# Performance work log

Measured on AMD Instinct MI355X. Metric: run time of the kernel, lower is better.

## Reference

```python
import jax, jax.numpy as jnp
import numpy as np

B, T, E, H = 8, 2048, 1024, 128

def setup_inputs() -> dict:
    key = jax.random.key(0)
    kx, kq, kk, kv = jax.random.split(key, 4)
    return {
        "X": jax.random.normal(kx, (B, T, E), dtype=jnp.float32),
        "Wq": jax.random.normal(kq, (E, H), dtype=jnp.float32) * (E ** -0.5),
        "Wk": jax.random.normal(kk, (E, H), dtype=jnp.float32) * (E ** -0.5),
        "Wv": jax.random.normal(kv, (E, H), dtype=jnp.float32) * (E ** -0.5),
    }

def reference(X, Wq, Wk, Wv):
    # X: [B, T, E]; Wq/Wk/Wv: [E, H]
    q = X @ Wq  # [B, T, H]
    k = X @ Wk  # [B, T, H]
    v = X @ Wv  # [B, T, H]
    t = X.shape[1]
    scale = float(X.shape[-1]) ** 0.5  # NOTE: source scales by sqrt(embedding_size)
    w = jnp.einsum("bqh,bkh->bqk", q, k) / scale  # [B, T, T]
    mask = jnp.tril(jnp.ones((t, t), dtype=bool))  # causal tril buffer
    w = jnp.where(mask[None, :, :], w, -jnp.inf)
    # NOTE: source applies softmax over dim=1 (the query axis), faithfully reproduced
    w = jax.nn.softmax(w, axis=1)
    # dropout p=0.0 -> identity
    return jnp.einsum("bqk,bkh->bqh", w, v)  # [B, T, H]
```

## Files before the change

### kernel.cpp

```cpp
#include <hip/hip_runtime.h>
#include <hip/hip_bf16.h>
#include <stdint.h>

#define B_ 8
#define T_ 2048
#define E_ 1024
#define H_ 128
#define BT_ (B_*T_)

typedef unsigned short u16;
typedef unsigned int u32;
typedef __attribute__((ext_vector_type(4))) unsigned short u16x4;
typedef __attribute__((ext_vector_type(8))) short short8;
typedef __attribute__((ext_vector_type(4))) float f32x4;

#define MFMA_BF16(a,b,c) __builtin_amdgcn_mfma_f32_16x16x32_bf16((a),(b),(c),0,0,0)

__device__ __forceinline__ u16 bf16u(float f) {
  union { float f; unsigned u; } v; v.f = f;
  unsigned r = v.u + 0x7FFFu + ((v.u >> 16) & 1u);
  return (u16)(r >> 16);
}
__device__ __forceinline__ float ubf16(u16 u) {
  union { unsigned u; float f; } v; v.u = ((unsigned)u) << 16; return v.f;
}

__device__ __forceinline__ void gl16(const void* g, void* l) {
  __builtin_amdgcn_global_load_lds(
      (const __attribute__((address_space(1))) void*)g,
      (__attribute__((address_space(3))) void*)l, 16, 0, 0);
}

template<int R, int CB, bool SWZ>
__device__ __forceinline__ void stage_tile(const char* g, int gstride, char* lds) {
  const int lane = threadIdx.x & 63;
  const int wid  = threadIdx.x >> 6;
  constexpr int LPR   = CB / 16;
  constexpr int RPC   = 1024 / CB;
  constexpr int CALLS = (R * CB) / 1024;
  constexpr int CPW   = CALLS / 4;
#pragma unroll
  for (int c = 0; c < CPW; ++c) {
    const int call = wid * CPW + c;
    const int r0   = call * RPC;
    const int row  = r0 + lane / LPR;
    int s = lane % LPR;
    if (SWZ) s = s ^ (row & 7);
    gl16(g + (size_t)row * gstride + s * 16, lds + (size_t)r0 * CB);
  }
}

__device__ __forceinline__ short8 fragr(const u16* lds, int row, int colu16, int CBu) {
  const int slot = (colu16 >> 3) ^ (row & 7);
  return *(const short8*)&lds[(size_t)row * CBu + (slot << 3)];
}

__global__ void k_convert_x(const float* __restrict__ X, u16* __restrict__ Xb) {
  const int n4 = BT_ * E_ / 4;
  for (int i = blockIdx.x * 256 + threadIdx.x; i < n4; i += gridDim.x * 256) {
    float4 v = ((const float4*)X)[i];
    u16x4 o;
    o.x = bf16u(v.x); o.y = bf16u(v.y); o.z = bf16u(v.z); o.w = bf16u(v.w);
    ((u16x4*)Xb)[i] = o;
  }
}

__global__ void k_build_wt(const float* __restrict__ Wq, const float* __restrict__ Wk,
                           const float* __restrict__ Wv, u16* __restrict__ Wt) {
  int idx = blockIdx.x * 256 + threadIdx.x;
  if (idx >= 384 * 1024) return;
  int r = idx >> 10;
  int e = idx & 1023;
  int i = r >> 7;
  int h = r & 127;
  const float* W = (i == 0) ? Wq : (i == 1) ? Wk : Wv;
  float v = W[(size_t)e * 128 + h];
  if (i == 0) v *= 0.03125f;
  Wt[idx] = bf16u(v);
}

__global__ __launch_bounds__(256) void k_qkv_gemm(const u16* __restrict__ Xb, const u16* __restrict__ Wt,
                                                  u16* __restrict__ Qs, u16* __restrict__ Kb,
                                                  u16* __restrict__ Vt) {
  __shared__ __align__(16) u16 As[128 * 64];
  __shared__ __align__(16) u16 Bs[128 * 64];
  const int m0   = blockIdx.x * 128;
  const int nsel = blockIdx.y;
  const int n0   = nsel * 128;
  const int lane = threadIdx.x & 63;
  const int wid  = threadIdx.x >> 6;
  const int ln = lane & 15, hi = lane >> 4;
  const int wm = (wid >> 1) * 64, wn = (wid & 1) * 64;
  f32x4 acc[4][4] = {};
  for (int ks = 0; ks < E_; ks += 64) {
    stage_tile<128, 128, true>((const char*)(Xb + (size_t)m0 * E_ + ks), E_ * 2, (char*)As);
    stage_tile<128, 128, true>((const char*)(Wt + (size_t)n0 * E_ + ks), E_ * 2, (char*)Bs);
    __syncthreads();
#pragma unroll
    for (int kk = 0; kk < 2; ++kk) {
      short8 a[4], b[4];
#pragma unroll
      for (int mf = 0; mf < 4; ++mf)
        a[mf] = fragr(As, wm + mf * 16 + ln, kk * 32 + hi * 8, 64);
#pragma unroll
      for (int nf = 0; nf < 4; ++nf)
        b[nf] = fragr(Bs, wn + nf * 16 + ln, kk * 32 + hi * 8, 64);
#pragma unroll
      for (int mf = 0; mf < 4; ++mf)
#pragma unroll
        for (int nf = 0; nf < 4; ++nf)
          acc[mf][nf] = MFMA_BF16(a[mf], b[nf], acc[mf][nf]);
    }
    __syncthreads();
  }
#pragma unroll
  for (int mf = 0; mf < 4; ++mf)
#pragma unroll
    for (int nf = 0; nf < 4; ++nf)
#pragma unroll
      for (int i = 0; i < 4; ++i) {
        int r = m0 + wm + mf * 16 + hi * 4 + i;
        int c = wn + nf * 16 + ln;
        u16 u = bf16u(acc[mf][nf][i]);
        if (nsel == 0)      Qs[(size_t)r * H_ + c] = u;
        else if (nsel == 1) Kb[(size_t)r * H_ + c] = u;
        else {
          int bb = r >> 11, t = r & (T_ - 1);
          Vt[((size_t)bb * H_ + c) * T_ + t] = u;
        }
      }
}

__global__ __launch_bounds__(256) void k_score(const u16* __restrict__ Qs, const u16* __restrict__ Kb,
                                               u16* __restrict__ P, float* __restrict__ colsum,
                                               int b_base) {
  __shared__ __align__(16) u16 QtPs[128 * 128];
  __shared__ __align__(16) u16 Ks[128 * 128];
  __shared__ float cs[128];
  const int tid = blockIdx.x;
  const int bl  = blockIdx.y;
  const int b   = b_base + bl;
  int qt = (int)((sqrtf(8.f * tid + 1.f) - 1.f) * 0.5f);
  while ((qt + 1) * (qt + 2) / 2 <= tid) ++qt;
  while (qt * (qt + 1) / 2 > tid) --qt;
  const int kt = tid - qt * (qt + 1) / 2;

  const int lane = threadIdx.x & 63, wid = threadIdx.x >> 6;
  const int ln = lane & 15, hi = lane >> 4;
  const int wq0 = wid * 32;

  stage_tile<128, 256, true>((const char*)(Qs + ((size_t)b * T_ + qt * 128) * H_), H_ * 2, (char*)QtPs);
  stage_tile<128, 256, true>((const char*)(Kb + ((size_t)b * T_ + kt * 128) * H_), H_ * 2, (char*)Ks);
  if (threadIdx.x < 128) cs[threadIdx.x] = 0.f;
  __syncthreads();

  f32x4 acc[2][8] = {};
#pragma unroll
  for (int kk = 0; kk < 4; ++kk) {
    short8 a[2], bf[8];
#pragma unroll
    for (int mf = 0; mf < 2; ++mf)
      a[mf] = fragr(QtPs, wq0 + mf * 16 + ln, kk * 32 + hi * 8, 128);
#pragma unroll
    for (int nf = 0; nf < 8; ++nf)
      bf[nf] = fragr(Ks, nf * 16 + ln, kk * 32 + hi * 8, 128);
#pragma unroll
    for (int mf = 0; mf < 2; ++mf)
#pragma unroll
      for (int nf = 0; nf < 8; ++nf)
        acc[mf][nf] = MFMA_BF16(a[mf], bf[nf], acc[mf][nf]);
  }

  const bool diag = (qt == kt);
#pragma unroll
  for (int nf = 0; nf < 8; ++nf) {
    float s = 0.f;
    const int k = nf * 16 + ln;
#pragma unroll
    for (int mf = 0; mf < 2; ++mf) {
#pragma unroll
      for (int i = 0; i < 4; ++i) {
        const int q = wq0 + mf * 16 + hi * 4 + i;
        float w = __expf(acc[mf][nf][i]);
        if (diag && q < k) w = 0.f;
        acc[mf][nf][i] = w;
        s += w;
      }
    }
    s += __shfl_xor(s, 16);
    s += __shfl_xor(s, 32);
    if (hi == 0) atomicAdd(&cs[nf * 16 + ln], s);
  }
  __syncthreads();

  u16* Ps = QtPs;
  const bool evenlane = !(ln & 1);
#pragma unroll
  for (int mf = 0; mf < 2; ++mf)
#pragma unroll
    for (int nf = 0; nf < 8; ++nf) {
      f32x4 v = acc[mf][nf];
      f32x4 pv;
#pragma unroll
      for (int i = 0; i < 4; ++i) pv[i] = __shfl_xor(v[i], 1);
#pragma unroll
      for (int j = 0; j < 2; ++j) {
        const int i = evenlane ? j : (2 + j);
        const float lo = evenlane ? v[i] : pv[i];
        const float hh = evenlane ? pv[i] : v[i];
        const u32 pk = (u32)bf16u(lo) | ((u32)bf16u(hh) << 16);
        const int row = wq0 + mf * 16 + hi * 4 + i;
        const int kc  = nf * 16 + (ln & ~1);
        const int byt = row * 256 + ((((kc >> 3) ^ (row & 7)) << 4) | ((kc & 7) << 1));
        *(u32*)((char*)Ps + byt) = pk;
      }
    }
  __syncthreads();

  u16* ptile = P + (((size_t)bl * 136 + tid) << 14);
#pragma unroll
  for (int pass = 0; pass < 8; ++pass) {
    const int row = pass * 16 + (threadIdx.x >> 4);
    const int s   = threadIdx.x & 15;
    short8 val = *(const short8*)&Ps[row * 128 + (((s ^ (row & 7)) << 3))];
    *(short8*)&ptile[row * 128 + s * 8] = val;
  }
  if (threadIdx.x < 128)
    atomicAdd(&colsum[(size_t)b * T_ + kt * 128 + threadIdx.x], cs[threadIdx.x]);
}

__global__ void k_finalize_v(const float* __restrict__ colsum, u16* __restrict__ Vt, int b_base) {
  const int i8 = blockIdx.x * 256 + threadIdx.x;
  const int bl = i8 >> 15;
  const int r  = i8 & 32767;
  const int h  = r >> 8;
  const int t8 = r & 255;
  const int b  = b_base + bl;
  u16* p = Vt + ((size_t)b * H_ + h) * T_ + t8 * 8;
  const float* csp = colsum + (size_t)b * T_ + t8 * 8;
  short8 v = *(short8*)p;
  short8 o;
#pragma unroll
  for (int j = 0; j < 8; ++j) {
    float f = ubf16((u16)v[j]) / csp[j];
    o[j] = (short)bf16u(f);
  }
  *(short8*)p = o;
}

__global__ __launch_bounds__(256) void k_pv(const u16* __restrict__ P, const u16* __restrict__ Vt,
                                            float* __restrict__ out, int b_base) {
  __shared__ __align__(16) u16 Pt[128 * 128];
  __shared__ __align__(16) u16 Vs[128 * 128];
  const int id = blockIdx.x;
  const int bl = blockIdx.y;
  const int b  = b_base + bl;
  int qt = 0, cum = 0;
#pragma unroll
  for (int j = 0; j < 16; ++j) {
    const int n = (j + 2) >> 1;
    if (id < cum + n) { qt = j; break; }
    cum += n;
  }
  const int c   = id - cum;
  const int nch = (qt + 2) >> 1;
  const int kt0 = c * (qt + 1) / nch;
  const int kt1 = (c + 1) * (qt + 1) / nch;

  const int lane = threadIdx.x & 63, wid = threadIdx.x >> 6;
  const int ln = lane & 15, hi = lane >> 4;
  const int wq0 = wid * 32;

  f32x4 acc[2][8] = {};
  for (int kt = kt0; kt < kt1; ++kt) {
    const u16* ptile = P + (((size_t)bl * 136 + (size_t)qt * (qt + 1) / 2 + kt) << 14);
    stage_tile<128, 256, true>((const char*)ptile, 256, (char*)Pt);
    stage_tile<128, 256, true>((const char*)(Vt + (size_t)b * H_ * T_ + kt * 128), T_ * 2, (char*)Vs);
    __syncthreads();
#pragma unroll
    for (int kk = 0; kk < 4; ++kk) {
      short8 a[2], bf[8];
#pragma unroll
      for (int mf = 0; mf < 2; ++mf)
        a[mf] = fragr(Pt, wq0 + mf * 16 + ln, kk * 32 + hi * 8, 128);
#pragma unroll
      for (int nf = 0; nf < 8; ++nf)
        bf[nf] = fragr(Vs, nf * 16 + ln, kk * 32 + hi * 8, 128);
#pragma unroll
      for (int mf = 0; mf < 2; ++mf)
#pragma unroll
        for (int nf = 0; nf < 8; ++nf)
          acc[mf][nf] = MFMA_BF16(a[mf], bf[nf], acc[mf][nf]);
    }
    __syncthreads();
  }
#pragma unroll
  for (int mf = 0; mf < 2; ++mf)
#pragma unroll
    for (int nf = 0; nf < 8; ++nf)
#pragma unroll
      for (int i = 0; i < 4; ++i) {
        const int q = qt * 128 + wq0 + mf * 16 + hi * 4 + i;
        const int h = nf * 16 + ln;
        atomicAdd(&out[((size_t)b * T_ + q) * H_ + h], acc[mf][nf][i]);
      }
}

extern "C" void kernel_launch(void* const* d_in, const int* in_sizes, int n_in,
                              void* d_out, int out_size, void* d_ws, size_t ws_size,
                              hipStream_t stream) {
  const float* X  = (const float*)d_in[0];
  const float* Wq = (const float*)d_in[1];
  const float* Wk = (const float*)d_in[2];
  const float* Wv = (const float*)d_in[3];
  float* out = (float*)d_out;
  char* ws = (char*)d_ws;

  u16*  Xb     = (u16*)(ws + 0);
  u16*  Wt     = (u16*)(ws + 33554432);
  u16*  Qs     = (u16*)(ws + 34340864);
  u16*  Kb     = (u16*)(ws + 38535168);
  u16*  Vt     = (u16*)(ws + 42729472);
  float* colsum = (float*)(ws + 46923776);
  int phases, nb;
  u16* Pb;
  if (ws_size >= 82640896ULL) { phases = 1; nb = 8; Pb = (u16*)(ws + 46989312); }
  else                        { phases = 2; nb = 4; Pb = (u16*)(ws + 0); }

  hipMemsetAsync(out, 0, (size_t)BT_ * H_ * sizeof(float), stream);
  hipMemsetAsync(colsum, 0, BT_ * sizeof(float), stream);
  k_convert_x<<<2048, 256, 0, stream>>>(X, Xb);
  k_build_wt<<<1536, 256, 0, stream>>>(Wq, Wk, Wv, Wt);
  k_qkv_gemm<<<dim3(128, 3), 256, 0, stream>>>(Xb, Wt, Qs, Kb, Vt);
  for (int p = 0; p < phases; ++p) {
    const int b_base = p * nb;
    k_score<<<dim3(136, nb), 256, 0, stream>>>(Qs, Kb, Pb, colsum, b_base);
    k_finalize_v<<<nb * 128, 256, 0, stream>>>(colsum, Vt, b_base);
    k_pv<<<dim3(72, nb), 256, 0, stream>>>(Pb, Vt, out, b_base);
  }
}
```

Before: 206.2 us.

## Restructure score and PV kernels with paired causal tiles and head-split PV

```diff
diff --git a/kernel.cpp b/kernel.cpp
--- a/kernel.cpp
+++ b/kernel.cpp
@@ -55,28 +55,27 @@
   return *(const short8*)&lds[(size_t)row * CBu + (slot << 3)];
 }
 
-__global__ void k_convert_x(const float* __restrict__ X, u16* __restrict__ Xb) {
+__global__ void k_prep(const float* __restrict__ X, u16* __restrict__ Xb,
+                       const float* __restrict__ Wq, const float* __restrict__ Wk,
+                       const float* __restrict__ Wv, u16* __restrict__ Wt) {
+  const int gidx = blockIdx.x * 256 + threadIdx.x;
   const int n4 = BT_ * E_ / 4;
-  for (int i = blockIdx.x * 256 + threadIdx.x; i < n4; i += gridDim.x * 256) {
+  for (int i = gidx; i < n4; i += gridDim.x * 256) {
     float4 v = ((const float4*)X)[i];
     u16x4 o;
     o.x = bf16u(v.x); o.y = bf16u(v.y); o.z = bf16u(v.z); o.w = bf16u(v.w);
     ((u16x4*)Xb)[i] = o;
   }
-}
-
-__global__ void k_build_wt(const float* __restrict__ Wq, const float* __restrict__ Wk,
-                           const float* __restrict__ Wv, u16* __restrict__ Wt) {
-  int idx = blockIdx.x * 256 + threadIdx.x;
-  if (idx >= 384 * 1024) return;
-  int r = idx >> 10;
-  int e = idx & 1023;
-  int i = r >> 7;
-  int h = r & 127;
-  const float* W = (i == 0) ? Wq : (i == 1) ? Wk : Wv;
-  float v = W[(size_t)e * 128 + h];
-  if (i == 0) v *= 0.03125f;
-  Wt[idx] = bf16u(v);
+  if (gidx < 384 * 1024) {
+    int r = gidx >> 10;
+    int e = gidx & 1023;
+    int i = r >> 7;
+    int h = r & 127;
+    const float* W = (i == 0) ? Wq : (i == 1) ? Wk : Wv;
+    float v = W[(size_t)e * 128 + h];
+    if (i == 0) v *= 0.03125f;
+    Wt[gidx] = bf16u(v);
+  }
 }
 
 __global__ __launch_bounds__(256) void k_qkv_gemm(const u16* __restrict__ Xb, const u16* __restrict__ Wt,
@@ -89,7 +88,7 @@
   const int n0   = nsel * 128;
   const int lane = threadIdx.x & 63;
   const int wid  = threadIdx.x >> 6;
-  const int ln = lane & 15, hi = lane >> 4;
+  const int ln = lane & 15, h4 = lane >> 4;
   const int wm = (wid >> 1) * 64, wn = (wid & 1) * 64;
   f32x4 acc[4][4] = {};
   for (int ks = 0; ks < E_; ks += 64) {
@@ -101,10 +100,10 @@
       short8 a[4], b[4];
 #pragma unroll
       for (int mf = 0; mf < 4; ++mf)
-        a[mf] = fragr(As, wm + mf * 16 + ln, kk * 32 + hi * 8, 64);
+        a[mf] = fragr(As, wm + mf * 16 + ln, kk * 32 + h4 * 8, 64);
 #pragma unroll
       for (int nf = 0; nf < 4; ++nf)
-        b[nf] = fragr(Bs, wn + nf * 16 + ln, kk * 32 + hi * 8, 64);
+        b[nf] = fragr(Bs, wn + nf * 16 + ln, kk * 32 + h4 * 8, 64);
 #pragma unroll
       for (int mf = 0; mf < 4; ++mf)
 #pragma unroll
@@ -119,7 +118,7 @@
     for (int nf = 0; nf < 4; ++nf)
 #pragma unroll
       for (int i = 0; i < 4; ++i) {
-        int r = m0 + wm + mf * 16 + hi * 4 + i;
+        int r = m0 + wm + mf * 16 + h4 * 4 + i;
         int c = wn + nf * 16 + ln;
         u16 u = bf16u(acc[mf][nf][i]);
         if (nsel == 0)      Qs[(size_t)r * H_ + c] = u;
@@ -132,110 +131,105 @@
 }
 
 __global__ __launch_bounds__(256) void k_score(const u16* __restrict__ Qs, const u16* __restrict__ Kb,
-                                               u16* __restrict__ P, float* __restrict__ colsum,
-                                               int b_base) {
-  __shared__ __align__(16) u16 QtPs[128 * 128];
-  __shared__ __align__(16) u16 Ks[128 * 128];
-  __shared__ float cs[128];
-  const int tid = blockIdx.x;
-  const int bl  = blockIdx.y;
-  const int b   = b_base + bl;
-  int qt = (int)((sqrtf(8.f * tid + 1.f) - 1.f) * 0.5f);
-  while ((qt + 1) * (qt + 2) / 2 <= tid) ++qt;
-  while (qt * (qt + 1) / 2 > tid) --qt;
-  const int kt = tid - qt * (qt + 1) / 2;
-
+                                               u16* __restrict__ P, float* __restrict__ colsum) {
+  __shared__ __align__(16) u16 Qb[128 * 128];
+  __shared__ __align__(16) u16 Kf[128 * 128];
+  const int c = blockIdx.x, a = blockIdx.y, b = blockIdx.z;
+  const int lo = (c * 17) >> 3, hi = ((c + 1) * 17) >> 3;
   const int lane = threadIdx.x & 63, wid = threadIdx.x >> 6;
-  const int ln = lane & 15, hi = lane >> 4;
+  const int ln = lane & 15, h4 = lane >> 4;
   const int wq0 = wid * 32;
-
-  stage_tile<128, 256, true>((const char*)(Qs + ((size_t)b * T_ + qt * 128) * H_), H_ * 2, (char*)QtPs);
-  stage_tile<128, 256, true>((const char*)(Kb + ((size_t)b * T_ + kt * 128) * H_), H_ * 2, (char*)Ks);
-  if (threadIdx.x < 128) cs[threadIdx.x] = 0.f;
-  __syncthreads();
-
-  f32x4 acc[2][8] = {};
-#pragma unroll
-  for (int kk = 0; kk < 4; ++kk) {
-    short8 a[2], bf[8];
+  const bool evenlane = !(ln & 1);
+  int curqt = -1;
+  for (int t = lo; t < hi; ++t) {
+    const int qt = (t <= a) ? a : 15 - a;
+    const int kt = (t <= a) ? t : t - (a + 1);
+    if (qt != curqt) {
+      stage_tile<128, 256, true>((const char*)(Qs + ((size_t)b * T_ + qt * 128) * H_), H_ * 2, (char*)Qb);
+      curqt = qt;
+    }
+    stage_tile<128, 256, true>((const char*)(Kb + ((size_t)b * T_ + kt * 128) * H_), H_ * 2, (char*)Kf);
+    __syncthreads();
+
+    f32x4 acc[2][8] = {};
+#pragma unroll
+    for (int kk = 0; kk < 4; ++kk) {
+      short8 av[2], bv[8];
+#pragma unroll
+      for (int mf = 0; mf < 2; ++mf)
+        av[mf] = fragr(Qb, wq0 + mf * 16 + ln, kk * 32 + h4 * 8, 128);
+#pragma unroll
+      for (int nf = 0; nf < 8; ++nf)
+        bv[nf] = fragr(Kf, nf * 16 + ln, kk * 32 + h4 * 8, 128);
+#pragma unroll
+      for (int mf = 0; mf < 2; ++mf)
+#pragma unroll
+        for (int nf = 0; nf < 8; ++nf)
+          acc[mf][nf] = MFMA_BF16(av[mf], bv[nf], acc[mf][nf]);
+    }
+
+    const bool diag = (qt == kt);
+#pragma unroll
+    for (int nf = 0; nf < 8; ++nf) {
+      float s = 0.f;
+      const int k = nf * 16 + ln;
+#pragma unroll
+      for (int mf = 0; mf < 2; ++mf) {
+#pragma unroll
+        for (int i = 0; i < 4; ++i) {
+          const int q = wq0 + mf * 16 + h4 * 4 + i;
+          float w = __expf(acc[mf][nf][i]);
+          if (diag && q < k) w = 0.f;
+          acc[mf][nf][i] = w;
+          s += w;
+        }
+      }
+      s += __shfl_xor(s, 16);
+      s += __shfl_xor(s, 32);
+      if (h4 == 0) atomicAdd(&colsum[(size_t)b * T_ + kt * 128 + nf * 16 + ln], s);
+    }
+    __syncthreads();
+
 #pragma unroll
     for (int mf = 0; mf < 2; ++mf)
-      a[mf] = fragr(QtPs, wq0 + mf * 16 + ln, kk * 32 + hi * 8, 128);
-#pragma unroll
-    for (int nf = 0; nf < 8; ++nf)
-      bf[nf] = fragr(Ks, nf * 16 + ln, kk * 32 + hi * 8, 128);
-#pragma unroll
-    for (int mf = 0; mf < 2; ++mf)
-#pragma unroll
-      for (int nf = 0; nf < 8; ++nf)
-        acc[mf][nf] = MFMA_BF16(a[mf], bf[nf], acc[mf][nf]);
-  }
-
-  const bool diag = (qt == kt);
-#pragma unroll
-  for (int nf = 0; nf < 8; ++nf) {
-    float s = 0.f;
-    const int k = nf * 16 + ln;
-#pragma unroll
-    for (int mf = 0; mf < 2; ++mf) {
-#pragma unroll
-      for (int i = 0; i < 4; ++i) {
-        const int q = wq0 + mf * 16 + hi * 4 + i;
-        float w = __expf(acc[mf][nf][i]);
-        if (diag && q < k) w = 0.f;
-        acc[mf][nf][i] = w;
-        s += w;
-      }
-    }
-    s += __shfl_xor(s, 16);
-    s += __shfl_xor(s, 32);
-    if (hi == 0) atomicAdd(&cs[nf * 16 + ln], s);
-  }
-  __syncthreads();
-
-  u16* Ps = QtPs;
-  const bool evenlane = !(ln & 1);
-#pragma unroll
-  for (int mf = 0; mf < 2; ++mf)
-#pragma unroll
-    for (int nf = 0; nf < 8; ++nf) {
-      f32x4 v = acc[mf][nf];
-      f32x4 pv;
-#pragma unroll
-      for (int i = 0; i < 4; ++i) pv[i] = __shfl_xor(v[i], 1);
-#pragma unroll
-      for (int j = 0; j < 2; ++j) {
-        const int i = evenlane ? j : (2 + j);
-        const float lo = evenlane ? v[i] : pv[i];
-        const float hh = evenlane ? pv[i] : v[i];
-        const u32 pk = (u32)bf16u(lo) | ((u32)bf16u(hh) << 16);
-        const int row = wq0 + mf * 16 + hi * 4 + i;
-        const int kc  = nf * 16 + (ln & ~1);
-        const int byt = row * 256 + ((((kc >> 3) ^ (row & 7)) << 4) | ((kc & 7) << 1));
-        *(u32*)((char*)Ps + byt) = pk;
-      }
-    }
-  __syncthreads();
-
-  u16* ptile = P + (((size_t)bl * 136 + tid) << 14);
-#pragma unroll
-  for (int pass = 0; pass < 8; ++pass) {
-    const int row = pass * 16 + (threadIdx.x >> 4);
-    const int s   = threadIdx.x & 15;
-    short8 val = *(const short8*)&Ps[row * 128 + (((s ^ (row & 7)) << 3))];
-    *(short8*)&ptile[row * 128 + s * 8] = val;
-  }
-  if (threadIdx.x < 128)
-    atomicAdd(&colsum[(size_t)b * T_ + kt * 128 + threadIdx.x], cs[threadIdx.x]);
-}
-
-__global__ void k_finalize_v(const float* __restrict__ colsum, u16* __restrict__ Vt, int b_base) {
+#pragma unroll
+      for (int nf = 0; nf < 8; ++nf) {
+        f32x4 v = acc[mf][nf];
+        f32x4 pv;
+#pragma unroll
+        for (int i = 0; i < 4; ++i) pv[i] = __shfl_xor(v[i], 1);
+#pragma unroll
+        for (int j = 0; j < 2; ++j) {
+          const int i = evenlane ? j : (2 + j);
+          const float flo = evenlane ? v[i] : pv[i];
+          const float fhh = evenlane ? pv[i] : v[i];
+          const u32 pk = (u32)bf16u(flo) | ((u32)bf16u(fhh) << 16);
+          const int row = wq0 + mf * 16 + h4 * 4 + i;
+          const int kc  = nf * 16 + (ln & ~1);
+          const int byt = row * 256 + ((((kc >> 3) ^ (row & 7)) << 4) | ((kc & 7) << 1));
+          *(u32*)((char*)Kf + byt) = pk;
+        }
+      }
+    __syncthreads();
+
+    u16* ptile = P + (((size_t)b * 136 + (size_t)qt * (qt + 1) / 2 + kt) << 14);
+#pragma unroll
+    for (int pass = 0; pass < 8; ++pass) {
+      const int row = pass * 16 + (threadIdx.x >> 4);
+      const int s   = threadIdx.x & 15;
+      short8 val = *(const short8*)&Kf[row * 128 + ((s ^ (row & 7)) << 3)];
+      *(short8*)&ptile[row * 128 + s * 8] = val;
+    }
+    __syncthreads();
+  }
+}
+
+__global__ void k_finalize_v(const float* __restrict__ colsum, u16* __restrict__ Vt) {
   const int i8 = blockIdx.x * 256 + threadIdx.x;
-  const int bl = i8 >> 15;
+  const int b  = i8 >> 15;
   const int r  = i8 & 32767;
   const int h  = r >> 8;
   const int t8 = r & 255;
-  const int b  = b_base + bl;
   u16* p = Vt + ((size_t)b * H_ + h) * T_ + t8 * 8;
   const float* csp = colsum + (size_t)b * T_ + t8 * 8;
   short8 v = *(short8*)p;
@@ -249,61 +243,44 @@
 }
 
 __global__ __launch_bounds__(256) void k_pv(const u16* __restrict__ P, const u16* __restrict__ Vt,
-                                            float* __restrict__ out, int b_base) {
+                                            float* __restrict__ out) {
   __shared__ __align__(16) u16 Pt[128 * 128];
-  __shared__ __align__(16) u16 Vs[128 * 128];
+  __shared__ __align__(16) u16 Vs[16 * 128];
   const int id = blockIdx.x;
-  const int bl = blockIdx.y;
-  const int b  = b_base + bl;
-  int qt = 0, cum = 0;
-#pragma unroll
-  for (int j = 0; j < 16; ++j) {
-    const int n = (j + 2) >> 1;
-    if (id < cum + n) { qt = j; break; }
-    cum += n;
-  }
-  const int c   = id - cum;
-  const int nch = (qt + 2) >> 1;
-  const int kt0 = c * (qt + 1) / nch;
-  const int kt1 = (c + 1) * (qt + 1) / nch;
-
+  const int hq = id >> 6;
+  const int b  = (id >> 3) & 7;
+  const int a  = id & 7;
   const int lane = threadIdx.x & 63, wid = threadIdx.x >> 6;
-  const int ln = lane & 15, hi = lane >> 4;
+  const int ln = lane & 15, h4 = lane >> 4;
   const int wq0 = wid * 32;
-
-  f32x4 acc[2][8] = {};
-  for (int kt = kt0; kt < kt1; ++kt) {
-    const u16* ptile = P + (((size_t)bl * 136 + (size_t)qt * (qt + 1) / 2 + kt) << 14);
-    stage_tile<128, 256, true>((const char*)ptile, 256, (char*)Pt);
-    stage_tile<128, 256, true>((const char*)(Vt + (size_t)b * H_ * T_ + kt * 128), T_ * 2, (char*)Vs);
-    __syncthreads();
-#pragma unroll
-    for (int kk = 0; kk < 4; ++kk) {
-      short8 a[2], bf[8];
-#pragma unroll
-      for (int mf = 0; mf < 2; ++mf)
-        a[mf] = fragr(Pt, wq0 + mf * 16 + ln, kk * 32 + hi * 8, 128);
-#pragma unroll
-      for (int nf = 0; nf < 8; ++nf)
-        bf[nf] = fragr(Vs, nf * 16 + ln, kk * 32 + hi * 8, 128);
-#pragma unroll
-      for (int mf = 0; mf < 2; ++mf)
-#pragma unroll
-        for (int nf = 0; nf < 8; ++nf)
-          acc[mf][nf] = MFMA_BF16(a[mf], bf[nf], acc[mf][nf]);
-    }
-    __syncthreads();
-  }
-#pragma unroll
-  for (int mf = 0; mf < 2; ++mf)
-#pragma unroll
-    for (int nf = 0; nf < 8; ++nf)
+#pragma unroll
+  for (int half = 0; half < 2; ++half) {
+    const int qt = half ? (15 - a) : a;
+    f32x4 acc[2] = {};
+    for (int kt = 0; kt <= qt; ++kt) {
+      const u16* ptile = P + (((size_t)b * 136 + (size_t)qt * (qt + 1) / 2 + kt) << 14);
+      stage_tile<128, 256, true>((const char*)ptile, 256, (char*)Pt);
+      stage_tile<16, 256, true>((const char*)(Vt + ((size_t)b * H_ + hq * 16) * T_ + kt * 128), T_ * 2, (char*)Vs);
+      __syncthreads();
+#pragma unroll
+      for (int kk = 0; kk < 4; ++kk) {
+        short8 bv = fragr(Vs, ln, kk * 32 + h4 * 8, 128);
+#pragma unroll
+        for (int mf = 0; mf < 2; ++mf) {
+          short8 av = fragr(Pt, wq0 + mf * 16 + ln, kk * 32 + h4 * 8, 128);
+          acc[mf] = MFMA_BF16(av, bv, acc[mf]);
+        }
+      }
+      __syncthreads();
+    }
+#pragma unroll
+    for (int mf = 0; mf < 2; ++mf)
 #pragma unroll
       for (int i = 0; i < 4; ++i) {
-        const int q = qt * 128 + wq0 + mf * 16 + hi * 4 + i;
-        const int h = nf * 16 + ln;
-        atomicAdd(&out[((size_t)b * T_ + q) * H_ + h], acc[mf][nf][i]);
-      }
+        const int q = qt * 128 + wq0 + mf * 16 + h4 * 4 + i;
+        out[((size_t)b * T_ + q) * H_ + hq * 16 + ln] = acc[mf][i];
+      }
+  }
 }
 
 extern "C" void kernel_launch(void* const* d_in, const int* in_sizes, int n_in,
@@ -316,26 +293,30 @@
   float* out = (float*)d_out;
   char* ws = (char*)d_ws;
 
-  u16*  Xb     = (u16*)(ws + 0);
-  u16*  Wt     = (u16*)(ws + 33554432);
-  u16*  Qs     = (u16*)(ws + 34340864);
-  u16*  Kb     = (u16*)(ws + 38535168);
-  u16*  Vt     = (u16*)(ws + 42729472);
-  float* colsum = (float*)(ws + 46923776);
-  int phases, nb;
-  u16* Pb;
-  if (ws_size >= 82640896ULL) { phases = 1; nb = 8; Pb = (u16*)(ws + 46989312); }
-  else                        { phases = 2; nb = 4; Pb = (u16*)(ws + 0); }
-
-  hipMemsetAsync(out, 0, (size_t)BT_ * H_ * sizeof(float), stream);
+  u16 *Xb, *Wt, *Qs, *Kb, *Vt, *Pb;
+  float* colsum;
+  if (ws_size >= 82640896ULL) {
+    Xb = (u16*)(ws + 0);
+    Wt = (u16*)(ws + 33554432);
+    Qs = (u16*)(ws + 34340864);
+    Kb = (u16*)(ws + 38535168);
+    Vt = (u16*)(ws + 42729472);
+    colsum = (float*)(ws + 46923776);
+    Pb = (u16*)(ws + 46989312);
+  } else {
+    Qs = (u16*)(ws + 0);
+    Kb = (u16*)(ws + 4194304);
+    Vt = (u16*)(ws + 8388608);
+    colsum = (float*)(ws + 12582912);
+    Pb = (u16*)(ws + 12648448);
+    Xb = (u16*)(ws + 12648448);
+    Wt = (u16*)(ws + 46202880);
+  }
+
   hipMemsetAsync(colsum, 0, BT_ * sizeof(float), stream);
-  k_convert_x<<<2048, 256, 0, stream>>>(X, Xb);
-  k_build_wt<<<1536, 256, 0, stream>>>(Wq, Wk, Wv, Wt);
+  k_prep<<<2048, 256, 0, stream>>>(X, Xb, Wq, Wk, Wv, Wt);
   k_qkv_gemm<<<dim3(128, 3), 256, 0, stream>>>(Xb, Wt, Qs, Kb, Vt);
-  for (int p = 0; p < phases; ++p) {
-    const int b_base = p * nb;
-    k_score<<<dim3(136, nb), 256, 0, stream>>>(Qs, Kb, Pb, colsum, b_base);
-    k_finalize_v<<<nb * 128, 256, 0, stream>>>(colsum, Vt, b_base);
-    k_pv<<<dim3(72, nb), 256, 0, stream>>>(Pb, Vt, out, b_base);
-  }
-}
+  k_score<<<dim3(8, 8, 8), 256, 0, stream>>>(Qs, Kb, Pb, colsum);
+  k_finalize_v<<<1024, 256, 0, stream>>>(colsum, Vt);
+  k_pv<<<512, 256, 0, stream>>>(Pb, Vt, out);
+}
```

After: 180.9 us. 1.14x faster.
